# Kernel tuning notes

Measured on AMD Instinct MI355X. Metric: run time of the kernel, lower is better.

The kernel has to match this reference:

```python
import jax, jax.numpy as jnp
import numpy as np
import math

RES = 1024
HEADS = 16
HEAD_RES = RES // HEADS
B, S = 2, 2048


def setup_inputs() -> dict:
    key = jax.random.key(0)
    kx, kq, kk, kv = jax.random.split(key, 4)
    scale = 1.0 / math.sqrt(RES)
    return {
        "x": jax.random.normal(kx, (B, S, RES), dtype=jnp.float32),
        "Wq": jax.random.normal(kq, (RES, RES), dtype=jnp.float32) * scale,
        "Wk": jax.random.normal(kk, (RES, RES), dtype=jnp.float32) * scale,
        "Wv": jax.random.normal(kv, (RES, RES), dtype=jnp.float32) * scale,
    }


def reference(x, Wq, Wk, Wv):
    batch, seq, _ = x.shape
    # projections (torch Linear without bias: x @ W.T; here W stored as [in, out])
    def split_heads(t):
        return t.reshape(batch, seq, HEADS, HEAD_RES).transpose(0, 2, 1, 3)  # [B,H,S,D]
    q = split_heads(x @ Wq)
    k = split_heads(x @ Wk)
    v = split_heads(x @ Wv)
    scores = jnp.einsum("bhsd,bhtd->bhst", q, k) / math.sqrt(HEAD_RES)
    attn = jax.nn.softmax(scores, axis=-1)
    out = jnp.einsum("bhst,bhtd->bhsd", attn, v)  # [B,H,S,D]
    return out.transpose(0, 2, 1, 3).reshape(batch, seq, RES)
```

## Files before the change

kernel.cpp:

```cpp
#include <hip/hip_runtime.h>

typedef _Float16 f16;
typedef _Float16 half8 __attribute__((ext_vector_type(8)));
typedef float f32x4 __attribute__((ext_vector_type(4)));
typedef unsigned int u32x4 __attribute__((ext_vector_type(4)));

#define RES 1024
#define NH 16
#define HD 64
#define BATCH 2
#define SEQ 2048
#define M_ROWS (BATCH * SEQ)

__device__ __forceinline__ void gload_lds16(const void* g, void* l) {
  __builtin_amdgcn_global_load_lds(
      (const __attribute__((address_space(1))) unsigned int*)g,
      (__attribute__((address_space(3))) unsigned int*)l, 16, 0, 0);
}

__device__ __forceinline__ unsigned pk16(float a, float b) {
  auto h = __builtin_amdgcn_cvt_pkrtz(a, b);
  return __builtin_bit_cast(unsigned, h);
}

__device__ __forceinline__ void swap32(unsigned a, unsigned b, unsigned& x, unsigned& y) {
#if __has_builtin(__builtin_amdgcn_permlane32_swap)
  auto t = __builtin_amdgcn_permlane32_swap(a, b, false, false);
  x = (unsigned)t[0];
  y = (unsigned)t[1];
#else
  unsigned ax = __shfl_xor(a, 32), bx = __shfl_xor(b, 32);
  int hi = (threadIdx.x & 63) >> 5;
  x = hi ? bx : a;
  y = hi ? b : ax;
#endif
}

__device__ __forceinline__ void swap16(unsigned a, unsigned b, unsigned& x, unsigned& y) {
#if __has_builtin(__builtin_amdgcn_permlane16_swap)
  auto t = __builtin_amdgcn_permlane16_swap(a, b, false, false);
  x = (unsigned)t[0];
  y = (unsigned)t[1];
#else
  unsigned ax = __shfl_xor(a, 16), bx = __shfl_xor(b, 16);
  int q1 = ((threadIdx.x & 63) >> 4) & 1;
  x = q1 ? bx : a;
  y = q1 ? b : ax;
#endif
}

__global__ __launch_bounds__(256) void xconv_kernel(const float* __restrict__ x,
                                                    f16* __restrict__ xh) {
  int idx = blockIdx.x * 256 + threadIdx.x;
  const float4* xv = (const float4*)x;
  float4 a = xv[idx * 2];
  float4 b = xv[idx * 2 + 1];
  half8 h;
  h[0] = (f16)a.x; h[1] = (f16)a.y; h[2] = (f16)a.z; h[3] = (f16)a.w;
  h[4] = (f16)b.x; h[5] = (f16)b.y; h[6] = (f16)b.z; h[7] = (f16)b.w;
  ((half8*)xh)[idx] = h;
}

__global__ __launch_bounds__(1024) void wtrans_kernel(const float* __restrict__ Wq,
                                                      const float* __restrict__ Wk,
                                                      const float* __restrict__ Wv,
                                                      f16* __restrict__ Wt) {
  const float* W = blockIdx.z == 0 ? Wq : (blockIdx.z == 1 ? Wk : Wv);
  f16* Wo = Wt + (size_t)blockIdx.z * RES * RES;
  __shared__ float tile[32][33];
  int n = blockIdx.x * 32 + threadIdx.x;
  int k = blockIdx.y * 32 + threadIdx.y;
  tile[threadIdx.y][threadIdx.x] = W[(size_t)k * RES + n];
  __syncthreads();
  int ko = blockIdx.y * 32 + threadIdx.x;
  int no = blockIdx.x * 32 + threadIdx.y;
  Wo[(size_t)no * RES + ko] = (f16)tile[threadIdx.x][threadIdx.y];
}

__global__ __launch_bounds__(256) void proj_gemm_kernel(const f16* __restrict__ xh,
                                                        const f16* __restrict__ Wt,
                                                        f16* __restrict__ Qh,
                                                        f16* __restrict__ Kh,
                                                        f16* __restrict__ Vt) {
  int proj = blockIdx.z;
  const f16* Bt = Wt + (size_t)proj * RES * RES;
  int m0 = blockIdx.x * 128;
  int n0 = blockIdx.y * 128;
  __shared__ alignas(16) f16 Als[128 * 32];
  __shared__ alignas(16) f16 Bls[128 * 32];
  int t = threadIdx.x, lane = t & 63, w = t >> 6;
  int l15 = lane & 15, quad = lane >> 4;
  int wm = w >> 1, wn = w & 1;

  f32x4 zero = {0.f, 0.f, 0.f, 0.f};
  f32x4 acc[4][4];
#pragma unroll
  for (int mt = 0; mt < 4; mt++)
#pragma unroll
    for (int nt = 0; nt < 4; nt++) acc[mt][nt] = zero;

  for (int k0 = 0; k0 < RES; k0 += 32) {
#pragma unroll
    for (int i = 0; i < 2; i++) {
      int wl = i * 256 + w * 64;
      int linear = wl + lane;
      int row = linear >> 2;
      int kk = (linear & 3) * 8;
      gload_lds16(xh + (size_t)(m0 + row) * RES + k0 + kk, &Als[wl * 8]);
      gload_lds16(Bt + (size_t)(n0 + row) * RES + k0 + kk, &Bls[wl * 8]);
    }
    __syncthreads();
    half8 af[4], bf[4];
#pragma unroll
    for (int mt = 0; mt < 4; mt++)
      af[mt] = *(const half8*)&Als[(wm * 64 + mt * 16 + l15) * 32 + quad * 8];
#pragma unroll
    for (int nt = 0; nt < 4; nt++)
      bf[nt] = *(const half8*)&Bls[(wn * 64 + nt * 16 + l15) * 32 + quad * 8];
#pragma unroll
    for (int mt = 0; mt < 4; mt++)
#pragma unroll
      for (int nt = 0; nt < 4; nt++)
        acc[mt][nt] = __builtin_amdgcn_mfma_f32_16x16x32_f16(af[mt], bf[nt], acc[mt][nt], 0, 0, 0);
    __syncthreads();
  }

#pragma unroll
  for (int mt = 0; mt < 4; mt++) {
#pragma unroll
    for (int nt = 0; nt < 4; nt++) {
#pragma unroll
      for (int r = 0; r < 4; r++) {
        int row = m0 + wm * 64 + mt * 16 + quad * 4 + r;
        int col = n0 + wn * 64 + nt * 16 + l15;
        f16 v = (f16)acc[mt][nt][r];
        int b = row >> 11, s = row & (SEQ - 1);
        int h = col >> 6, d = col & (HD - 1);
        size_t bh = (size_t)b * NH + h;
        if (proj == 0)
          Qh[(bh * SEQ + s) * HD + d] = v;
        else if (proj == 1)
          Kh[(bh * SEQ + s) * HD + d] = v;
        else
          Vt[(bh * HD + d) * SEQ + s] = v;
      }
    }
  }
}

__global__ __launch_bounds__(128, 3) void flash_kernel(const f16* __restrict__ Qh,
                                                       const f16* __restrict__ Kh,
                                                       const f16* __restrict__ Vt,
                                                       float* __restrict__ out) {
  int L = blockIdx.x;
  int xcd = L & 7, slot = L >> 3;
  int bh = ((slot >> 5) << 3) | xcd;
  int qt = slot & 31;
  int b = bh >> 4, h = bh & 15;
  int tid = threadIdx.x;
  int lane = tid & 63, w = tid >> 6;
  int l15 = lane & 15, quad = lane >> 4;
  int qrow0 = qt * 64 + w * 32;

  __shared__ alignas(16) f16 Kls[64 * 64];
  __shared__ alignas(16) f16 Vls[64 * 64];

  const f16* kbase = Kh + (size_t)bh * SEQ * HD;
  const f16* vbase = Vt + (size_t)bh * HD * SEQ;

  int srow = tid >> 3;
  int schunk = tid & 7;

  const f16* qptr = Qh + ((size_t)bh * SEQ + qrow0 + l15) * HD + quad * 8;
  half8 qf[2][2];
  qf[0][0] = *(const half8*)qptr;
  qf[0][1] = *(const half8*)(qptr + 32);
  qf[1][0] = *(const half8*)(qptr + 16 * HD);
  qf[1][1] = *(const half8*)(qptr + 16 * HD + 32);
#pragma unroll
  for (int q2 = 0; q2 < 2; q2++)
#pragma unroll
    for (int ks = 0; ks < 2; ks++)
#pragma unroll
      for (int j = 0; j < 8; j++) qf[q2][ks][j] *= (f16)0.125f;

  f32x4 zero = {0.f, 0.f, 0.f, 0.f};
  float l_acc[2] = {0.f, 0.f};
  f32x4 o[2][4];
#pragma unroll
  for (int q2 = 0; q2 < 2; q2++)
#pragma unroll
    for (int nt = 0; nt < 4; nt++) o[q2][nt] = zero;

  int swz0 = (quad ^ (l15 & 7)) * 8;
  int swz1 = ((quad + 4) ^ (l15 & 7)) * 8;

  auto stage = [&](int kv0) {
#pragma unroll
    for (int rd = 0; rd < 4; rd++) {
      int row = rd * 16 + srow;
      int pc = schunk ^ (row & 7);
      gload_lds16(kbase + ((size_t)(kv0 + row) << 6) + pc * 8,
                  &Kls[rd * 1024 + w * 512]);
      gload_lds16(vbase + ((size_t)row * SEQ) + kv0 + pc * 8,
                  &Vls[rd * 1024 + w * 512]);
    }
  };

  stage(0);

  for (int kv0 = 0; kv0 < SEQ; kv0 += 64) {
    __syncthreads();

    half8 kf0[4], kf1[4];
#pragma unroll
    for (int tt = 0; tt < 4; tt++) {
      int row = tt * 16 + l15;
      kf0[tt] = *(const half8*)&Kls[row * 64 + swz0];
      kf1[tt] = *(const half8*)&Kls[row * 64 + swz1];
    }

    half8 pa[2][2];
#pragma unroll
    for (int q2 = 0; q2 < 2; q2++) {
      f32x4 sc[4];
#pragma unroll
      for (int tt = 0; tt < 4; tt++) {
        sc[tt] = __builtin_amdgcn_mfma_f32_16x16x32_f16(kf0[tt], qf[q2][0], zero, 0, 0, 0);
        sc[tt] = __builtin_amdgcn_mfma_f32_16x16x32_f16(kf1[tt], qf[q2][1], sc[tt], 0, 0, 0);
      }
      float ps = 0.f;
#pragma unroll
      for (int tt = 0; tt < 4; tt++)
#pragma unroll
        for (int r = 0; r < 4; r++) { sc[tt][r] = __expf(sc[tt][r]); ps += sc[tt][r]; }
      ps += __shfl_xor(ps, 16);
      ps += __shfl_xor(ps, 32);
      l_acc[q2] += ps;

      unsigned wp[4][2];
#pragma unroll
      for (int tt = 0; tt < 4; tt++) {
        wp[tt][0] = pk16(sc[tt][0], sc[tt][1]);
        wp[tt][1] = pk16(sc[tt][2], sc[tt][3]);
      }
#pragma unroll
      for (int ks = 0; ks < 2; ks++) {
        u32x4 pw;
#pragma unroll
        for (int i = 0; i < 2; i++) {
          unsigned a, bb, x, y;
          swap32(wp[2 * ks][i], wp[2 * ks + 1][i], a, bb);
          swap16(a, bb, x, y);
          pw[i] = x;
          pw[2 + i] = y;
        }
        pa[q2][ks] = __builtin_bit_cast(half8, pw);
      }
    }

    half8 vf0[4], vf1[4];
#pragma unroll
    for (int nt = 0; nt < 4; nt++) {
      int row = nt * 16 + l15;
      vf0[nt] = *(const half8*)&Vls[row * 64 + swz0];
      vf1[nt] = *(const half8*)&Vls[row * 64 + swz1];
    }

    __syncthreads();

    if (kv0 + 64 < SEQ) stage(kv0 + 64);

#pragma unroll
    for (int q2 = 0; q2 < 2; q2++)
#pragma unroll
      for (int ks = 0; ks < 2; ks++)
#pragma unroll
        for (int nt = 0; nt < 4; nt++)
          o[q2][nt] = __builtin_amdgcn_mfma_f32_16x16x32_f16(pa[q2][ks], ks ? vf1[nt] : vf0[nt], o[q2][nt], 0, 0, 0);
  }

#pragma unroll
  for (int q2 = 0; q2 < 2; q2++) {
    float linv[4];
#pragma unroll
    for (int r = 0; r < 4; r++) linv[r] = 1.0f / __shfl(l_acc[q2], quad * 4 + r);
#pragma unroll
    for (int nt = 0; nt < 4; nt++) {
#pragma unroll
      for (int r = 0; r < 4; r++) {
        int s = qrow0 + q2 * 16 + quad * 4 + r;
        out[((size_t)b * SEQ + s) * RES + h * HD + nt * 16 + l15] = o[q2][nt][r] * linv[r];
      }
    }
  }
}

extern "C" void kernel_launch(void* const* d_in, const int* in_sizes, int n_in,
                              void* d_out, int out_size, void* d_ws, size_t ws_size,
                              hipStream_t stream) {
  (void)in_sizes; (void)n_in; (void)out_size; (void)ws_size;
  const float* x  = (const float*)d_in[0];
  const float* Wq = (const float*)d_in[1];
  const float* Wk = (const float*)d_in[2];
  const float* Wv = (const float*)d_in[3];
  float* out = (float*)d_out;

  f16* xh = (f16*)d_ws;
  f16* Wt = xh + (size_t)M_ROWS * RES;
  f16* Qh = Wt + (size_t)3 * RES * RES;
  f16* Kh = Qh + (size_t)BATCH * NH * SEQ * HD;
  f16* Vt = Kh + (size_t)BATCH * NH * SEQ * HD;

  xconv_kernel<<<M_ROWS * RES / (256 * 8), 256, 0, stream>>>(x, xh);
  wtrans_kernel<<<dim3(32, 32, 3), dim3(32, 32), 0, stream>>>(Wq, Wk, Wv, Wt);
  proj_gemm_kernel<<<dim3(M_ROWS / 128, RES / 128, 3), 256, 0, stream>>>(xh, Wt, Qh, Kh, Vt);
  flash_kernel<<<1024, 128, 0, stream>>>(Qh, Kh, Vt, out);
}
```

Before: 169.3 us.

## Double-buffer K/V LDS tiles and raise wave priority around MFMA blocks

Converts the K/V shared-memory tiles to double buffers so the next tile's global-to-LDS load is issued at the start of each iteration, and one of the two barriers per iteration is removed. This gives the loads a whole iteration of compute to hide behind. It also wraps the MFMA sections in s_setprio to favour matrix issue across waves. The cost is doubled LDS use (32KB per block), which may reduce occupancy below the 3-block launch bound.

```diff
diff --git a/kernel.cpp b/kernel.cpp
--- a/kernel.cpp
+++ b/kernel.cpp
@@ -162,8 +162,8 @@
   int l15 = lane & 15, quad = lane >> 4;
   int qrow0 = qt * 64 + w * 32;
 
-  __shared__ alignas(16) f16 Kls[64 * 64];
-  __shared__ alignas(16) f16 Vls[64 * 64];
+  __shared__ alignas(16) f16 Kls[2][64 * 64];
+  __shared__ alignas(16) f16 Vls[2][64 * 64];
 
   const f16* kbase = Kh + (size_t)bh * SEQ * HD;
   const f16* vbase = Vt + (size_t)bh * HD * SEQ;
@@ -195,40 +195,48 @@
   int swz0 = (quad ^ (l15 & 7)) * 8;
   int swz1 = ((quad + 4) ^ (l15 & 7)) * 8;
 
-  auto stage = [&](int kv0) {
+  auto stage = [&](int kv0, int pb) {
 #pragma unroll
     for (int rd = 0; rd < 4; rd++) {
       int row = rd * 16 + srow;
       int pc = schunk ^ (row & 7);
       gload_lds16(kbase + ((size_t)(kv0 + row) << 6) + pc * 8,
-                  &Kls[rd * 1024 + w * 512]);
+                  &Kls[pb][rd * 1024 + w * 512]);
       gload_lds16(vbase + ((size_t)row * SEQ) + kv0 + pc * 8,
-                  &Vls[rd * 1024 + w * 512]);
+                  &Vls[pb][rd * 1024 + w * 512]);
     }
   };
 
-  stage(0);
-
-  for (int kv0 = 0; kv0 < SEQ; kv0 += 64) {
+  stage(0, 0);
+
+  constexpr int NT = SEQ / 64;
+  for (int it = 0; it < NT; ++it) {
+    int buf = it & 1;
     __syncthreads();
+    if (it + 1 < NT) stage((it + 1) * 64, buf ^ 1);
+
+    const f16* Kb = &Kls[buf][0];
+    const f16* Vb = &Vls[buf][0];
 
     half8 kf0[4], kf1[4];
 #pragma unroll
     for (int tt = 0; tt < 4; tt++) {
       int row = tt * 16 + l15;
-      kf0[tt] = *(const half8*)&Kls[row * 64 + swz0];
-      kf1[tt] = *(const half8*)&Kls[row * 64 + swz1];
+      kf0[tt] = *(const half8*)&Kb[row * 64 + swz0];
+      kf1[tt] = *(const half8*)&Kb[row * 64 + swz1];
     }
 
     half8 pa[2][2];
 #pragma unroll
     for (int q2 = 0; q2 < 2; q2++) {
       f32x4 sc[4];
+      __builtin_amdgcn_s_setprio(1);
 #pragma unroll
       for (int tt = 0; tt < 4; tt++) {
         sc[tt] = __builtin_amdgcn_mfma_f32_16x16x32_f16(kf0[tt], qf[q2][0], zero, 0, 0, 0);
         sc[tt] = __builtin_amdgcn_mfma_f32_16x16x32_f16(kf1[tt], qf[q2][1], sc[tt], 0, 0, 0);
       }
+      __builtin_amdgcn_s_setprio(0);
       float ps = 0.f;
 #pragma unroll
       for (int tt = 0; tt < 4; tt++)
@@ -263,14 +271,11 @@
 #pragma unroll
     for (int nt = 0; nt < 4; nt++) {
       int row = nt * 16 + l15;
-      vf0[nt] = *(const half8*)&Vls[row * 64 + swz0];
-      vf1[nt] = *(const half8*)&Vls[row * 64 + swz1];
-    }
-
-    __syncthreads();
-
-    if (kv0 + 64 < SEQ) stage(kv0 + 64);
-
+      vf0[nt] = *(const half8*)&Vb[row * 64 + swz0];
+      vf1[nt] = *(const half8*)&Vb[row * 64 + swz1];
+    }
+
+    __builtin_amdgcn_s_setprio(1);
 #pragma unroll
     for (int q2 = 0; q2 < 2; q2++)
 #pragma unroll
@@ -278,6 +283,7 @@
 #pragma unroll
         for (int nt = 0; nt < 4; nt++)
           o[q2][nt] = __builtin_amdgcn_mfma_f32_16x16x32_f16(pa[q2][ks], ks ? vf1[nt] : vf0[nt], o[q2][nt], 0, 0, 0);
+    __builtin_amdgcn_s_setprio(0);
   }
 
 #pragma unroll
```

New measurement: 172.1 us. No clear change (+1.7%).

## Double-buffer projection GEMM LDS tiles and swizzle blocks for XCD L2 locality

Applied to the files above, without the earlier changes.

The projection GEMM now keeps two LDS buffers for the A and B tiles. It issues the direct-to-LDS global loads for the next K step right after reading the current fragments into registers, which lets one barrier per iteration replace two and overlaps loads with MFMA work. The 3D grid is flattened to 768 blocks and remapped so that blocks landing on the same XCD under round-robin dispatch get consecutive tiles sharing one weight slice, which is meant to improve L2 reuse. LDS use doubles. Correctness relies on the barrier waiting for the outstanding async LDS loads.

```diff
diff --git a/kernel.cpp b/kernel.cpp
--- a/kernel.cpp
+++ b/kernel.cpp
@@ -82,12 +82,17 @@
                                                         f16* __restrict__ Qh,
                                                         f16* __restrict__ Kh,
                                                         f16* __restrict__ Vt) {
-  int proj = blockIdx.z;
+  int flat = blockIdx.x;
+  int swz = (flat & 7) * 96 + (flat >> 3);
+  int mb = swz & 31;
+  int rest = swz >> 5;
+  int nb = rest & 7;
+  int proj = rest >> 3;
   const f16* Bt = Wt + (size_t)proj * RES * RES;
-  int m0 = blockIdx.x * 128;
-  int n0 = blockIdx.y * 128;
-  __shared__ alignas(16) f16 Als[128 * 32];
-  __shared__ alignas(16) f16 Bls[128 * 32];
+  int m0 = mb * 128;
+  int n0 = nb * 128;
+  __shared__ alignas(16) f16 Als[2][128 * 32];
+  __shared__ alignas(16) f16 Bls[2][128 * 32];
   int t = threadIdx.x, lane = t & 63, w = t >> 6;
   int l15 = lane & 15, quad = lane >> 4;
   int wm = w >> 1, wn = w & 1;
@@ -99,30 +104,40 @@
 #pragma unroll
     for (int nt = 0; nt < 4; nt++) acc[mt][nt] = zero;
 
-  for (int k0 = 0; k0 < RES; k0 += 32) {
+  auto stageAB = [&](int k0, int pb) {
 #pragma unroll
     for (int i = 0; i < 2; i++) {
       int wl = i * 256 + w * 64;
       int linear = wl + lane;
       int row = linear >> 2;
       int kk = (linear & 3) * 8;
-      gload_lds16(xh + (size_t)(m0 + row) * RES + k0 + kk, &Als[wl * 8]);
-      gload_lds16(Bt + (size_t)(n0 + row) * RES + k0 + kk, &Bls[wl * 8]);
-    }
+      gload_lds16(xh + (size_t)(m0 + row) * RES + k0 + kk, &Als[pb][wl * 8]);
+      gload_lds16(Bt + (size_t)(n0 + row) * RES + k0 + kk, &Bls[pb][wl * 8]);
+    }
+  };
+
+  stageAB(0, 0);
+
+  constexpr int KSTEPS = RES / 32;
+  for (int it = 0; it < KSTEPS; ++it) {
+    int pb = it & 1;
     __syncthreads();
+
     half8 af[4], bf[4];
 #pragma unroll
     for (int mt = 0; mt < 4; mt++)
-      af[mt] = *(const half8*)&Als[(wm * 64 + mt * 16 + l15) * 32 + quad * 8];
+      af[mt] = *(const half8*)&Als[pb][(wm * 64 + mt * 16 + l15) * 32 + quad * 8];
 #pragma unroll
     for (int nt = 0; nt < 4; nt++)
-      bf[nt] = *(const half8*)&Bls[(wn * 64 + nt * 16 + l15) * 32 + quad * 8];
+      bf[nt] = *(const half8*)&Bls[pb][(wn * 64 + nt * 16 + l15) * 32 + quad * 8];
+
+    if (it + 1 < KSTEPS) stageAB((it + 1) * 32, pb ^ 1);
+
 #pragma unroll
     for (int mt = 0; mt < 4; mt++)
 #pragma unroll
       for (int nt = 0; nt < 4; nt++)
         acc[mt][nt] = __builtin_amdgcn_mfma_f32_16x16x32_f16(af[mt], bf[nt], acc[mt][nt], 0, 0, 0);
-    __syncthreads();
   }
 
 #pragma unroll
@@ -314,6 +329,6 @@
 
   xconv_kernel<<<M_ROWS * RES / (256 * 8), 256, 0, stream>>>(x, xh);
   wtrans_kernel<<<dim3(32, 32, 3), dim3(32, 32), 0, stream>>>(Wq, Wk, Wv, Wt);
-  proj_gemm_kernel<<<dim3(M_ROWS / 128, RES / 128, 3), 256, 0, stream>>>(xh, Wt, Qh, Kh, Vt);
+  proj_gemm_kernel<<<768, 256, 0, stream>>>(xh, Wt, Qh, Kh, Vt);
   flash_kernel<<<1024, 128, 0, stream>>>(Qh, Kh, Vt, out);
 }
```

New measurement: 185.1 us. +9.4%, slower.

## Merge x-convert and weight-transpose kernels and vectorize transposed V stores

Applied to the files above, without the earlier changes.

The separate x fp32->fp16 conversion and weight transpose kernels become one prep kernel, with the transpose now using 256-thread blocks. In the projection GEMM epilogue for V, accumulators are packed to fp16 pairs and rearranged across lanes with permlane swaps, so each lane writes a 16-byte contiguous chunk of the transposed V instead of scattered 2-byte stores. This targets one kernel launch and the strided single-element V writes, at the cost of extra cross-lane shuffles.

```diff
diff --git a/kernel.cpp b/kernel.cpp
--- a/kernel.cpp
+++ b/kernel.cpp
@@ -21,6 +21,12 @@
 __device__ __forceinline__ unsigned pk16(float a, float b) {
   auto h = __builtin_amdgcn_cvt_pkrtz(a, b);
   return __builtin_bit_cast(unsigned, h);
+}
+
+__device__ __forceinline__ unsigned pk16_rne(float a, float b) {
+  unsigned short la = __builtin_bit_cast(unsigned short, (f16)a);
+  unsigned short hb = __builtin_bit_cast(unsigned short, (f16)b);
+  return (unsigned)la | ((unsigned)hb << 16);
 }
 
 __device__ __forceinline__ void swap32(unsigned a, unsigned b, unsigned& x, unsigned& y) {
@@ -49,32 +55,40 @@
 #endif
 }
 
-__global__ __launch_bounds__(256) void xconv_kernel(const float* __restrict__ x,
-                                                    f16* __restrict__ xh) {
-  int idx = blockIdx.x * 256 + threadIdx.x;
-  const float4* xv = (const float4*)x;
-  float4 a = xv[idx * 2];
-  float4 b = xv[idx * 2 + 1];
-  half8 h;
-  h[0] = (f16)a.x; h[1] = (f16)a.y; h[2] = (f16)a.z; h[3] = (f16)a.w;
-  h[4] = (f16)b.x; h[5] = (f16)b.y; h[6] = (f16)b.z; h[7] = (f16)b.w;
-  ((half8*)xh)[idx] = h;
-}
-
-__global__ __launch_bounds__(1024) void wtrans_kernel(const float* __restrict__ Wq,
-                                                      const float* __restrict__ Wk,
-                                                      const float* __restrict__ Wv,
-                                                      f16* __restrict__ Wt) {
-  const float* W = blockIdx.z == 0 ? Wq : (blockIdx.z == 1 ? Wk : Wv);
-  f16* Wo = Wt + (size_t)blockIdx.z * RES * RES;
+__global__ __launch_bounds__(256) void prep_kernel(const float* __restrict__ x,
+                                                   const float* __restrict__ Wq,
+                                                   const float* __restrict__ Wk,
+                                                   const float* __restrict__ Wv,
+                                                   f16* __restrict__ xh,
+                                                   f16* __restrict__ Wt) {
   __shared__ float tile[32][33];
-  int n = blockIdx.x * 32 + threadIdx.x;
-  int k = blockIdx.y * 32 + threadIdx.y;
-  tile[threadIdx.y][threadIdx.x] = W[(size_t)k * RES + n];
-  __syncthreads();
-  int ko = blockIdx.y * 32 + threadIdx.x;
-  int no = blockIdx.x * 32 + threadIdx.y;
-  Wo[(size_t)no * RES + ko] = (f16)tile[threadIdx.x][threadIdx.y];
+  int bid = blockIdx.x;
+  int tid = threadIdx.x;
+  if (bid < 2048) {
+    int idx = bid * 256 + tid;
+    const float4* xv = (const float4*)x;
+    float4 a = xv[idx * 2];
+    float4 b = xv[idx * 2 + 1];
+    half8 h;
+    h[0] = (f16)a.x; h[1] = (f16)a.y; h[2] = (f16)a.z; h[3] = (f16)a.w;
+    h[4] = (f16)b.x; h[5] = (f16)b.y; h[6] = (f16)b.z; h[7] = (f16)b.w;
+    ((half8*)xh)[idx] = h;
+  } else {
+    int wb = bid - 2048;
+    int bz = wb >> 10;
+    int rem = wb & 1023;
+    int by = rem >> 5, bx = rem & 31;
+    const float* W = bz == 0 ? Wq : (bz == 1 ? Wk : Wv);
+    f16* Wo = Wt + (size_t)bz * RES * RES;
+    int tx = tid & 31, ty = tid >> 5;
+#pragma unroll
+    for (int i = 0; i < 4; i++)
+      tile[ty + i * 8][tx] = W[(size_t)(by * 32 + ty + i * 8) * RES + bx * 32 + tx];
+    __syncthreads();
+#pragma unroll
+    for (int i = 0; i < 4; i++)
+      Wo[(size_t)(bx * 32 + ty + i * 8) * RES + by * 32 + tx] = (f16)tile[tx][ty + i * 8];
+  }
 }
 
 __global__ __launch_bounds__(256) void proj_gemm_kernel(const f16* __restrict__ xh,
@@ -125,24 +139,54 @@
     __syncthreads();
   }
 
-#pragma unroll
-  for (int mt = 0; mt < 4; mt++) {
+  if (proj == 2) {
+    int rowb = m0 + wm * 64;
+    int b = rowb >> 11;
+    int sbase = rowb & (SEQ - 1);
+    int h = (n0 + wn * 64) >> 6;
+    size_t bh = (size_t)b * NH + h;
 #pragma unroll
     for (int nt = 0; nt < 4; nt++) {
-#pragma unroll
-      for (int r = 0; r < 4; r++) {
-        int row = m0 + wm * 64 + mt * 16 + quad * 4 + r;
-        int col = n0 + wn * 64 + nt * 16 + l15;
-        f16 v = (f16)acc[mt][nt][r];
-        int b = row >> 11, s = row & (SEQ - 1);
-        int h = col >> 6, d = col & (HD - 1);
-        size_t bh = (size_t)b * NH + h;
-        if (proj == 0)
-          Qh[(bh * SEQ + s) * HD + d] = v;
-        else if (proj == 1)
-          Kh[(bh * SEQ + s) * HD + d] = v;
-        else
-          Vt[(bh * HD + d) * SEQ + s] = v;
+      unsigned wp[4][2];
+#pragma unroll
+      for (int mt = 0; mt < 4; mt++) {
+        wp[mt][0] = pk16_rne(acc[mt][nt][0], acc[mt][nt][1]);
+        wp[mt][1] = pk16_rne(acc[mt][nt][2], acc[mt][nt][3]);
+      }
+#pragma unroll
+      for (int ks = 0; ks < 2; ks++) {
+        u32x4 pw;
+#pragma unroll
+        for (int i = 0; i < 2; i++) {
+          unsigned a, bb, xx, yy;
+          swap32(wp[2 * ks][i], wp[2 * ks + 1][i], a, bb);
+          swap16(a, bb, xx, yy);
+          pw[i] = xx;
+          pw[2 + i] = yy;
+        }
+        int d = nt * 16 + l15;
+        int s0 = sbase + ks * 32 + quad * 8;
+        *(half8*)&Vt[(bh * HD + d) * SEQ + s0] = __builtin_bit_cast(half8, pw);
+      }
+    }
+  } else {
+#pragma unroll
+    for (int mt = 0; mt < 4; mt++) {
+#pragma unroll
+      for (int nt = 0; nt < 4; nt++) {
+#pragma unroll
+        for (int r = 0; r < 4; r++) {
+          int row = m0 + wm * 64 + mt * 16 + quad * 4 + r;
+          int col = n0 + wn * 64 + nt * 16 + l15;
+          f16 v = (f16)acc[mt][nt][r];
+          int b = row >> 11, s = row & (SEQ - 1);
+          int h = col >> 6, d = col & (HD - 1);
+          size_t bh = (size_t)b * NH + h;
+          if (proj == 0)
+            Qh[(bh * SEQ + s) * HD + d] = v;
+          else
+            Kh[(bh * SEQ + s) * HD + d] = v;
+        }
       }
     }
   }
@@ -312,8 +356,7 @@
   f16* Kh = Qh + (size_t)BATCH * NH * SEQ * HD;
   f16* Vt = Kh + (size_t)BATCH * NH * SEQ * HD;
 
-  xconv_kernel<<<M_ROWS * RES / (256 * 8), 256, 0, stream>>>(x, xh);
-  wtrans_kernel<<<dim3(32, 32, 3), dim3(32, 32), 0, stream>>>(Wq, Wk, Wv, Wt);
+  prep_kernel<<<2048 + 3072, 256, 0, stream>>>(x, Wq, Wk, Wv, xh, Wt);
   proj_gemm_kernel<<<dim3(M_ROWS / 128, RES / 128, 3), 256, 0, stream>>>(xh, Wt, Qh, Kh, Vt);
   flash_kernel<<<1024, 128, 0, stream>>>(Qh, Kh, Vt, out);
 }
```

New measurement: 167.1 us. No clear change (-1.2%).
